# Optimization experiments

Measured on AMD Instinct MI355X. Metric: run time of the kernel, lower is better.

Reference implementation:

```python
import jax, jax.numpy as jnp
import numpy as np

B, S, D, H, DFF = 8, 1024, 1024, 16, 4096
DK = D // H
EPS = 1e-6
NEG = -1e9


def setup_inputs() -> dict:
    key = jax.random.key(0)
    ks = jax.random.split(key, 8)
    x = jax.random.normal(ks[0], (B, S, D), dtype=jnp.float32)
    mask = jnp.ones((B, 1, 1, S), dtype=jnp.int32)
    s = 0.02
    wq = jax.random.normal(ks[1], (D, D), jnp.float32) * s
    wk = jax.random.normal(ks[2], (D, D), jnp.float32) * s
    wv = jax.random.normal(ks[3], (D, D), jnp.float32) * s
    wo = jax.random.normal(ks[4], (D, D), jnp.float32) * s
    bq = jnp.zeros((D,), jnp.float32); bk = jnp.zeros((D,), jnp.float32)
    bv = jnp.zeros((D,), jnp.float32); bo = jnp.zeros((D,), jnp.float32)
    w1 = jax.random.normal(ks[5], (D, DFF), jnp.float32) * s
    b1 = jnp.zeros((DFF,), jnp.float32)
    w2 = jax.random.normal(ks[6], (DFF, D), jnp.float32) * s
    b2 = jnp.zeros((D,), jnp.float32)
    g1 = jnp.array(1.0, jnp.float32); be1 = jnp.array(0.0, jnp.float32)
    g2 = jnp.array(1.0, jnp.float32); be2 = jnp.array(0.0, jnp.float32)
    return dict(x=x, mask=mask, wq=wq, bq=bq, wk=wk, bk=bk, wv=wv, bv=bv,
                wo=wo, bo=bo, w1=w1, b1=b1, w2=w2, b2=b2,
                g1=g1, be1=be1, g2=g2, be2=be2)


def layer_norm(x, gamma, beta):
    # repo quirk: unbiased std (ddof=1), scalar gamma/beta, divide by (std+eps)
    mean = jnp.mean(x, axis=-1, keepdims=True)
    std = jnp.std(x, axis=-1, keepdims=True, ddof=1)
    return gamma * (x - mean) / (std + EPS) + beta


def mha(x, mask, wq, bq, wk, bk, wv, bv, wo, bo):
    q = (x @ wq + bq).reshape(B, S, H, DK).transpose(0, 2, 1, 3)  # bhsd
    k = (x @ wk + bk).reshape(B, S, H, DK).transpose(0, 2, 1, 3)
    v = (x @ wv + bv).reshape(B, S, H, DK).transpose(0, 2, 1, 3)
    scores = jnp.einsum('bhqd,bhkd->bhqk', q, k) / jnp.sqrt(jnp.float32(DK))
    scores = jnp.where(mask == 0, NEG, scores)
    attn = jax.nn.softmax(scores, axis=-1)
    out = jnp.einsum('bhqk,bhkd->bhqd', attn, v)
    out = out.transpose(0, 2, 1, 3).reshape(B, S, D)
    return out @ wo + bo


def reference(x, mask, wq, bq, wk, bk, wv, bv, wo, bo, w1, b1, w2, b2, g1, be1, g2, be2):
    # pre-LN residual: x + sublayer(norm(x)); dropout inert at eval
    x = x + mha(layer_norm(x, g1, be1), mask, wq, bq, wk, bk, wv, bv, wo, bo)
    h = layer_norm(x, g2, be2)
    x = x + (jax.nn.relu(h @ w1 + b1) @ w2 + b2)
    return x
```

## Files before the change

### kernel.cpp

```cpp
#include <hip/hip_runtime.h>
#include <math.h>

typedef __bf16 bf16;
typedef float f32x4 __attribute__((ext_vector_type(4)));
typedef bf16 bf16x8 __attribute__((ext_vector_type(8)));
typedef bf16 bf16x4 __attribute__((ext_vector_type(4)));

#define DEV __device__ __forceinline__

constexpr int Ss = 1024, Dd = 1024;
constexpr float EPSf = 1e-6f;
constexpr float SM_SCALE = 0.125f * 1.4426950408889634f;

DEV void gl_lds16(const void* g, void* l) {
  __builtin_amdgcn_global_load_lds(
      (const __attribute__((address_space(1))) void*)g,
      (__attribute__((address_space(3))) void*)l, 16, 0, 0);
}

__global__ __launch_bounds__(256) void transpose6_k(
    const float* __restrict__ i0, const float* __restrict__ i1,
    const float* __restrict__ i2, const float* __restrict__ i3,
    const float* __restrict__ i4, const float* __restrict__ i5,
    bf16* __restrict__ o0, bf16* __restrict__ o1, bf16* __restrict__ o2,
    bf16* __restrict__ o3, bf16* __restrict__ o4, bf16* __restrict__ o5) {
  __shared__ float t[64 * 65];
  const int bi = blockIdx.x;
  const float* in;
  bf16* out;
  int R, C, local, sh;
  if (bi < 1024) {
    const int j = bi >> 8;
    local = bi & 255; R = 1024; C = 1024; sh = 4;
    in = (j == 0) ? i0 : (j == 1) ? i1 : (j == 2) ? i2 : i3;
    out = (j == 0) ? o0 : (j == 1) ? o1 : (j == 2) ? o2 : o3;
  } else if (bi < 2048) {
    local = bi - 1024; R = 1024; C = 4096; sh = 6; in = i4; out = o4;
  } else {
    local = bi - 2048; R = 4096; C = 1024; sh = 4; in = i5; out = o5;
  }
  const int nx = 1 << sh;
  const int bx = local & (nx - 1), by = local >> sh;
  const int tid = threadIdx.x;
  const int tx = tid & 63, ty = tid >> 6;
  const int r0 = by * 64, c0 = bx * 64;
#pragma unroll
  for (int i = 0; i < 16; i++) {
    int r = ty + i * 4;
    t[r * 65 + tx] = in[(size_t)(r0 + r) * C + c0 + tx];
  }
  __syncthreads();
#pragma unroll
  for (int i = 0; i < 16; i++) {
    int r = ty + i * 4;
    out[(size_t)(c0 + r) * R + r0 + tx] = (bf16)t[tx * 65 + r];
  }
}

__global__ __launch_bounds__(256) void ln_kernel(
    const float* __restrict__ in, bf16* __restrict__ out,
    const float* __restrict__ gp, const float* __restrict__ bp) {
  const int row = blockIdx.x;
  const int tid = threadIdx.x;
  float v[4];
  const float* p = in + (size_t)row * Dd + tid * 4;
#pragma unroll
  for (int i = 0; i < 4; i++) v[i] = p[i];
  float s = v[0] + v[1] + v[2] + v[3];
  float s2 = v[0] * v[0] + v[1] * v[1] + v[2] * v[2] + v[3] * v[3];
#pragma unroll
  for (int m = 1; m < 64; m <<= 1) {
    s += __shfl_xor(s, m, 64);
    s2 += __shfl_xor(s2, m, 64);
  }
  __shared__ float ls[4], ls2[4];
  if ((tid & 63) == 0) {
    ls[tid >> 6] = s;
    ls2[tid >> 6] = s2;
  }
  __syncthreads();
  s = ls[0] + ls[1] + ls[2] + ls[3];
  s2 = ls2[0] + ls2[1] + ls2[2] + ls2[3];
  float mean = s * (1.0f / Dd);
  float var = (s2 - (float)Dd * mean * mean) * (1.0f / (Dd - 1));
  var = fmaxf(var, 0.0f);
  float g = gp[0], be = bp[0];
  float rs = g / (sqrtf(var) + EPSf);
  bf16* q = out + (size_t)row * Dd + tid * 4;
#pragma unroll
  for (int i = 0; i < 4; i++) q[i] = (bf16)((v[i] - mean) * rs + be);
}

template <int EPI, int BK>
__global__ __launch_bounds__(256) void gemm_bt(
    const bf16* __restrict__ A, const bf16* __restrict__ Bt,
    const float* __restrict__ bias, const float* __restrict__ bias2,
    const float* __restrict__ bias3, const float* __restrict__ resid,
    bf16* __restrict__ vtb, void* __restrict__ Cout, int M, int N, int K,
    int sa, int sb) {
  __shared__ __attribute__((aligned(16))) bf16 As[128 * BK];
  __shared__ __attribute__((aligned(16))) bf16 Bs[128 * BK];
  constexpr int CPR = BK / 8;
  constexpr int RPJ = 256 / CPR;
  constexpr int NJ = BK / 16;
  const int tid = threadIdx.x;
  const int ln = tid & 63;
  const int wv = tid >> 6;
  const int wm = wv >> 1, wn = wv & 1;
  const int quad = ln >> 4, l16 = ln & 15;
  const int l7 = l16 & 7;
  const int m0 = blockIdx.y * 128, n0 = blockIdx.x * 128;

  f32x4 acc[4][4];
#pragma unroll
  for (int i = 0; i < 4; i++)
#pragma unroll
    for (int j = 0; j < 4; j++) acc[i][j] = {0.f, 0.f, 0.f, 0.f};

  const int sr = tid / CPR;
  const int sc = (tid & (CPR - 1)) ^ (sr & 7);
  const size_t abase = (size_t)(m0 + sr) * sa + sc * 8;
  const size_t bbase = (size_t)(n0 + sr) * sb + sc * 8;

  for (int k0 = 0; k0 < K; k0 += BK) {
#pragma unroll
    for (int j = 0; j < NJ; j++) {
      gl_lds16(A + abase + (size_t)(j * RPJ) * sa + k0,
               (char*)As + j * 4096 + wv * 1024);
      gl_lds16(Bt + bbase + (size_t)(j * RPJ) * sb + k0,
               (char*)Bs + j * 4096 + wv * 1024);
    }
    __syncthreads();
#pragma unroll
    for (int kh = 0; kh < BK / 32; kh++) {
      bf16x8 af[4], bfr[4];
#pragma unroll
      for (int mi = 0; mi < 4; mi++)
        af[mi] = *(const bf16x8*)&As[(wm * 64 + mi * 16 + l16) * BK +
                                     ((kh * 4 + quad) ^ l7) * 8];
#pragma unroll
      for (int ni = 0; ni < 4; ni++)
        bfr[ni] = *(const bf16x8*)&Bs[(wn * 64 + ni * 16 + l16) * BK +
                                      ((kh * 4 + quad) ^ l7) * 8];
#pragma unroll
      for (int mi = 0; mi < 4; mi++)
#pragma unroll
        for (int ni = 0; ni < 4; ni++)
          acc[mi][ni] = __builtin_amdgcn_mfma_f32_16x16x32_bf16(
              af[mi], bfr[ni], acc[mi][ni], 0, 0, 0);
    }
    __syncthreads();
  }

#pragma unroll
  for (int mi = 0; mi < 4; mi++) {
    const int m = m0 + wm * 64 + mi * 16 + quad * 4;
#pragma unroll
    for (int ni = 0; ni < 4; ni++) {
      const int n = n0 + wn * 64 + ni * 16 + l16;
      float bvl;
      if constexpr (EPI == 4) {
        const int seg = n >> 10;
        const float* bp = (seg == 0) ? bias : (seg == 1) ? bias2 : bias3;
        bvl = bp[n & 1023];
      } else if constexpr (EPI == 3) {
        bvl = 0.0f;
      } else {
        bvl = bias[n];
      }
      if constexpr (EPI == 4) {
        if (n < 2048) {
#pragma unroll
          for (int r = 0; r < 4; r++)
            ((bf16*)Cout)[(size_t)(m + r) * N + n] =
                (bf16)(acc[mi][ni][r] + bvl);
        } else {
          bf16x4 tv;
#pragma unroll
          for (int r = 0; r < 4; r++) tv[r] = (bf16)(acc[mi][ni][r] + bvl);
          const size_t vrow = (size_t)((m >> 10) * 1024 + (n - 2048));
          *(bf16x4*)&vtb[vrow * Ss + (m & 1023)] = tv;
        }
      } else {
#pragma unroll
        for (int r = 0; r < 4; r++) {
          float val = acc[mi][ni][r] + bvl;
          const size_t idx = (size_t)(m + r) * N + n;
          if constexpr (EPI == 1) {
            ((float*)Cout)[idx] = val + resid[idx];
          } else if constexpr (EPI == 2) {
            ((bf16*)Cout)[idx] = (bf16)fmaxf(val, 0.0f);
          } else {
            ((float*)Cout)[idx] = val + resid[idx];
          }
        }
      }
    }
  }
}

__global__ __launch_bounds__(256) void attn_k(
    const bf16* __restrict__ qkv, const bf16* __restrict__ vt,
    const int* __restrict__ mask, bf16* __restrict__ ctx) {
  __shared__ __attribute__((aligned(16))) bf16 Qs[128 * 64];
  __shared__ __attribute__((aligned(16))) bf16 Ks[64 * 64];
  __shared__ __attribute__((aligned(16))) bf16 Vs[64 * 64];
  __shared__ __attribute__((aligned(16))) bf16 Ps[4 * 32 * 64];
  __shared__ float Fm[1024];
  const int tid = threadIdx.x;
  const int ln = tid & 63, w = tid >> 6;
  const int quad = ln >> 4, l16 = ln & 15;
  const int l7 = l16 & 7;
  const int bh = blockIdx.y;
  const int b = bh >> 4, h = bh & 15;
  const int q0 = blockIdx.x * 128;
  const int sr = tid >> 3;
  const int sc = (tid & 7) ^ (sr & 7);

  {
    const int4 mv = *(const int4*)&mask[b * Ss + tid * 4];
    const float ninf = -__builtin_inff();
    Fm[tid * 4 + 0] = mv.x ? 0.0f : ninf;
    Fm[tid * 4 + 1] = mv.y ? 0.0f : ninf;
    Fm[tid * 4 + 2] = mv.z ? 0.0f : ninf;
    Fm[tid * 4 + 3] = mv.w ? 0.0f : ninf;
  }
  {
#pragma unroll
    for (int j = 0; j < 4; j++) {
      const size_t ga =
          (size_t)(b * Ss + q0 + j * 32 + sr) * 3072 + h * 64 + sc * 8;
      gl_lds16(qkv + ga, (char*)Qs + j * 4096 + w * 1024);
    }
  }
  __syncthreads();
  bf16x8 aq[2][2];
#pragma unroll
  for (int qi = 0; qi < 2; qi++)
#pragma unroll
    for (int c = 0; c < 2; c++)
      aq[qi][c] = *(const bf16x8*)&Qs[(w * 32 + qi * 16 + l16) * 64 +
                                      ((c * 4 + quad) ^ l7) * 8];

  f32x4 o[2][4];
#pragma unroll
  for (int qi = 0; qi < 2; qi++)
#pragma unroll
    for (int i = 0; i < 4; i++) o[qi][i] = {0.f, 0.f, 0.f, 0.f};
  f32x4 psum[2] = {{0.f, 0.f, 0.f, 0.f}, {0.f, 0.f, 0.f, 0.f}};

  for (int kk0 = 0; kk0 < Ss; kk0 += 64) {
    {
#pragma unroll
      for (int j = 0; j < 2; j++) {
        const size_t ga = (size_t)(b * Ss + kk0 + j * 32 + sr) * 3072 + 1024 +
                          h * 64 + sc * 8;
        gl_lds16(qkv + ga, (char*)Ks + j * 4096 + w * 1024);
        const size_t gv = (size_t)(bh * 64 + j * 32 + sr) * Ss + kk0 + sc * 8;
        gl_lds16(vt + gv, (char*)Vs + j * 4096 + w * 1024);
      }
    }
    __syncthreads();

    f32x4 st[2][4];
#pragma unroll
    for (int nt = 0; nt < 4; nt++) {
      bf16x8 bk0 = *(const bf16x8*)&Ks[(nt * 16 + l16) * 64 + (quad ^ l7) * 8];
      bf16x8 bk1 =
          *(const bf16x8*)&Ks[(nt * 16 + l16) * 64 + ((4 + quad) ^ l7) * 8];
#pragma unroll
      for (int qi = 0; qi < 2; qi++) {
        f32x4 s = {0.f, 0.f, 0.f, 0.f};
        s = __builtin_amdgcn_mfma_f32_16x16x32_bf16(aq[qi][0], bk0, s, 0, 0, 0);
        s = __builtin_amdgcn_mfma_f32_16x16x32_bf16(aq[qi][1], bk1, s, 0, 0, 0);
        st[qi][nt] = s;
      }
    }
    float fmv[4];
#pragma unroll
    for (int nt = 0; nt < 4; nt++) fmv[nt] = Fm[kk0 + nt * 16 + l16];
#pragma unroll
    for (int qi = 0; qi < 2; qi++)
#pragma unroll
      for (int nt = 0; nt < 4; nt++)
#pragma unroll
        for (int r = 0; r < 4; r++) {
          const float p = exp2f(fmaf(st[qi][nt][r], SM_SCALE, fmv[nt]));
          st[qi][nt][r] = p;
          psum[qi][r] += p;
        }
#pragma unroll
    for (int qi = 0; qi < 2; qi++)
#pragma unroll
      for (int nt = 0; nt < 4; nt++) {
        const int ch = nt * 2 + (l16 >> 3);
#pragma unroll
        for (int r = 0; r < 4; r++) {
          const int pr = qi * 16 + quad * 4 + r;
          Ps[w * 2048 + pr * 64 + (ch ^ (pr & 7)) * 8 + l7] =
              (bf16)st[qi][nt][r];
        }
      }
#pragma unroll
    for (int kh = 0; kh < 2; kh++) {
      bf16x8 bv[4];
#pragma unroll
      for (int dt = 0; dt < 4; dt++)
        bv[dt] = *(const bf16x8*)&Vs[(dt * 16 + l16) * 64 +
                                     ((kh * 4 + quad) ^ l7) * 8];
#pragma unroll
      for (int qi = 0; qi < 2; qi++) {
        bf16x8 ap = *(const bf16x8*)&Ps[w * 2048 + (qi * 16 + l16) * 64 +
                                        ((kh * 4 + quad) ^ l7) * 8];
#pragma unroll
        for (int dt = 0; dt < 4; dt++)
          o[qi][dt] =
              __builtin_amdgcn_mfma_f32_16x16x32_bf16(ap, bv[dt], o[qi][dt],
                                                      0, 0, 0);
      }
    }
    __syncthreads();
  }
#pragma unroll
  for (int qi = 0; qi < 2; qi++)
#pragma unroll
    for (int r = 0; r < 4; r++) {
      float s = psum[qi][r];
#pragma unroll
      for (int m = 1; m < 16; m <<= 1) s += __shfl_xor(s, m, 64);
      psum[qi][r] = s;
    }
#pragma unroll
  for (int qi = 0; qi < 2; qi++) {
    const float inv0 = 1.0f / psum[qi][0], inv1 = 1.0f / psum[qi][1];
    const float inv2 = 1.0f / psum[qi][2], inv3 = 1.0f / psum[qi][3];
#pragma unroll
    for (int dt = 0; dt < 4; dt++) {
      const size_t base =
          (size_t)(b * Ss + q0 + w * 32 + qi * 16 + quad * 4) * Dd + h * 64 +
          dt * 16 + l16;
      ctx[base] = (bf16)(o[qi][dt][0] * inv0);
      ctx[base + Dd] = (bf16)(o[qi][dt][1] * inv1);
      ctx[base + 2 * Dd] = (bf16)(o[qi][dt][2] * inv2);
      ctx[base + 3 * Dd] = (bf16)(o[qi][dt][3] * inv3);
    }
  }
}

extern "C" void kernel_launch(void* const* d_in, const int* in_sizes, int n_in,
                              void* d_out, int out_size, void* d_ws,
                              size_t ws_size, hipStream_t stream) {
  (void)in_sizes; (void)n_in; (void)out_size;
  const float* x = (const float*)d_in[0];
  const int* mask = (const int*)d_in[1];
  const float* wq = (const float*)d_in[2];
  const float* bq = (const float*)d_in[3];
  const float* wk = (const float*)d_in[4];
  const float* bk = (const float*)d_in[5];
  const float* wvw = (const float*)d_in[6];
  const float* bv = (const float*)d_in[7];
  const float* wo = (const float*)d_in[8];
  const float* bo = (const float*)d_in[9];
  const float* w1 = (const float*)d_in[10];
  const float* b1 = (const float*)d_in[11];
  const float* w2 = (const float*)d_in[12];
  const float* b2 = (const float*)d_in[13];
  const float* g1 = (const float*)d_in[14];
  const float* be1 = (const float*)d_in[15];
  const float* g2 = (const float*)d_in[16];
  const float* be2 = (const float*)d_in[17];
  float* out = (float*)d_out;

  char* ws = (char*)d_ws;
  const size_t MB = 1024 * 1024;
  bf16* w1T = (bf16*)(ws + 0 * MB);
  bf16* w2T = (bf16*)(ws + 8 * MB);
  bf16* wqkvT = (bf16*)(ws + 16 * MB);
  bf16* woT = (bf16*)(ws + 22 * MB);
  bf16* lnb = (bf16*)(ws + 24 * MB);
  bf16* qkv = (bf16*)(ws + 40 * MB);
  bf16* vtb = (bf16*)(ws + 88 * MB);
  float* x1 = (float*)(ws + 40 * MB);
  bf16* ctx = lnb;

  dim3 blk(256);
  transpose6_k<<<3072, blk, 0, stream>>>(
      wq, wk, wvw, wo, w1, w2, wqkvT, wqkvT + (size_t)1024 * 1024,
      wqkvT + (size_t)2048 * 1024, woT, w1T, w2T);
  ln_kernel<<<8192, blk, 0, stream>>>(x, lnb, g1, be1);
  gemm_bt<4, 64><<<dim3(24, 64), blk, 0, stream>>>(
      lnb, wqkvT, bq, bk, bv, nullptr, vtb, qkv, 8192, 3072, 1024, 1024, 1024);
  attn_k<<<dim3(8, 128), blk, 0, stream>>>(qkv, vtb, mask, ctx);
  gemm_bt<1, 128><<<dim3(8, 64), blk, 0, stream>>>(
      ctx, woT, bo, nullptr, nullptr, x, nullptr, x1, 8192, 1024, 1024, 1024,
      1024);
  ln_kernel<<<8192, blk, 0, stream>>>(x1, lnb, g2, be2);

  if (ws_size >= 136 * MB) {
    bf16* mid = (bf16*)(ws + 72 * MB);
    gemm_bt<2, 64><<<dim3(32, 64), blk, 0, stream>>>(
        lnb, w1T, b1, nullptr, nullptr, nullptr, nullptr, mid, 8192, 4096,
        1024, 1024, 1024);
    gemm_bt<1, 128><<<dim3(8, 64), blk, 0, stream>>>(
        mid, w2T, b2, nullptr, nullptr, x1, nullptr, out, 8192, 1024, 4096,
        4096, 4096);
  } else {
    bf16* mid = (bf16*)(ws + 72 * MB);
    gemm_bt<2, 64><<<dim3(16, 64), blk, 0, stream>>>(
        lnb, w1T, b1, nullptr, nullptr, nullptr, nullptr, mid, 8192, 2048,
        1024, 1024, 1024);
    gemm_bt<1, 128><<<dim3(8, 64), blk, 0, stream>>>(
        mid, w2T, b2, nullptr, nullptr, x1, nullptr, out, 8192, 1024, 2048,
        2048, 4096);
    gemm_bt<2, 64><<<dim3(16, 64), blk, 0, stream>>>(
        lnb, w1T + (size_t)2048 * 1024, b1 + 2048, nullptr, nullptr, nullptr,
        nullptr, mid, 8192, 2048, 1024, 1024, 1024);
    gemm_bt<3, 128><<<dim3(8, 64), blk, 0, stream>>>(
        mid, w2T + 2048, nullptr, nullptr, nullptr, out, nullptr, out, 8192,
        1024, 2048, 2048, 4096);
  }
}
```

Measured before the change: 510.5 us.

## Stage V-transpose through LDS, compute softmax sum via MFMA, alias attention LDS

The QKV GEMM epilogue for the V segment now writes tiles into swizzled shared memory and then stores coalesced 16-byte rows of the transposed V, replacing scattered 8-byte stores. In attention, the row sum of probabilities is computed with an extra MFMA against a ones vector over the bf16 P tile, removing per-element adds and the final cross-lane shuffle reduction. This also makes the sum match the rounded P actually used. Attention shared memory is merged into one buffer with P aliased over Q to shrink the LDS footprint, and the Q load is issued before the mask setup. The risks are an extra barrier in the GEMM epilogue and a larger MFMA count.

```diff
diff --git a/kernel.cpp b/kernel.cpp
--- a/kernel.cpp
+++ b/kernel.cpp
@@ -98,8 +98,9 @@
     const float* __restrict__ bias3, const float* __restrict__ resid,
     bf16* __restrict__ vtb, void* __restrict__ Cout, int M, int N, int K,
     int sa, int sb) {
-  __shared__ __attribute__((aligned(16))) bf16 As[128 * BK];
-  __shared__ __attribute__((aligned(16))) bf16 Bs[128 * BK];
+  __shared__ __attribute__((aligned(16))) char smem[2 * 128 * BK * 2];
+  bf16* As = (bf16*)smem;
+  bf16* Bs = (bf16*)(smem + 128 * BK * 2);
   constexpr int CPR = BK / 8;
   constexpr int RPJ = 256 / CPR;
   constexpr int NJ = BK / 16;
@@ -152,36 +153,57 @@
     __syncthreads();
   }
 
-#pragma unroll
-  for (int mi = 0; mi < 4; mi++) {
-    const int m = m0 + wm * 64 + mi * 16 + quad * 4;
-#pragma unroll
-    for (int ni = 0; ni < 4; ni++) {
-      const int n = n0 + wn * 64 + ni * 16 + l16;
-      float bvl;
-      if constexpr (EPI == 4) {
-        const int seg = n >> 10;
-        const float* bp = (seg == 0) ? bias : (seg == 1) ? bias2 : bias3;
-        bvl = bp[n & 1023];
-      } else if constexpr (EPI == 3) {
-        bvl = 0.0f;
-      } else {
-        bvl = bias[n];
-      }
-      if constexpr (EPI == 4) {
-        if (n < 2048) {
+  if constexpr (EPI == 4) {
+    if (n0 < 2048) {
+#pragma unroll
+      for (int mi = 0; mi < 4; mi++) {
+        const int m = m0 + wm * 64 + mi * 16 + quad * 4;
+#pragma unroll
+        for (int ni = 0; ni < 4; ni++) {
+          const int n = n0 + wn * 64 + ni * 16 + l16;
+          const float bvl = (n < 1024) ? bias[n] : bias2[n - 1024];
 #pragma unroll
           for (int r = 0; r < 4; r++)
             ((bf16*)Cout)[(size_t)(m + r) * N + n] =
                 (bf16)(acc[mi][ni][r] + bvl);
-        } else {
+        }
+      }
+    } else {
+      bf16* T = (bf16*)smem;
+#pragma unroll
+      for (int mi = 0; mi < 4; mi++) {
+        const int ml = wm * 64 + mi * 16 + quad * 4;
+        const int c = ml >> 3, hf = (ml >> 2) & 1;
+#pragma unroll
+        for (int ni = 0; ni < 4; ni++) {
+          const int nl = wn * 64 + ni * 16 + l16;
+          const float bvl = bias3[(n0 - 2048) + nl];
           bf16x4 tv;
 #pragma unroll
           for (int r = 0; r < 4; r++) tv[r] = (bf16)(acc[mi][ni][r] + bvl);
-          const size_t vrow = (size_t)((m >> 10) * 1024 + (n - 2048));
-          *(bf16x4*)&vtb[vrow * Ss + (m & 1023)] = tv;
+          *(bf16x4*)&T[nl * 128 + ((c ^ (nl & 15)) << 3) + (hf << 2)] = tv;
         }
-      } else {
+      }
+      __syncthreads();
+      const size_t vbase =
+          ((size_t)(m0 >> 10) * 1024 + (n0 - 2048)) * Ss + (m0 & 1023);
+#pragma unroll
+      for (int p = 0; p < 8; p++) {
+        const int row = p * 16 + (tid >> 4);
+        const int k = tid & 15;
+        bf16x8 vv = *(const bf16x8*)&T[row * 128 + ((k ^ (row & 15)) << 3)];
+        *(bf16x8*)&vtb[vbase + (size_t)row * Ss + k * 8] = vv;
+      }
+    }
+  } else {
+#pragma unroll
+    for (int mi = 0; mi < 4; mi++) {
+      const int m = m0 + wm * 64 + mi * 16 + quad * 4;
+#pragma unroll
+      for (int ni = 0; ni < 4; ni++) {
+        const int n = n0 + wn * 64 + ni * 16 + l16;
+        float bvl = 0.0f;
+        if constexpr (EPI != 3) bvl = bias[n];
 #pragma unroll
         for (int r = 0; r < 4; r++) {
           float val = acc[mi][ni][r] + bvl;
@@ -202,11 +224,12 @@
 __global__ __launch_bounds__(256) void attn_k(
     const bf16* __restrict__ qkv, const bf16* __restrict__ vt,
     const int* __restrict__ mask, bf16* __restrict__ ctx) {
-  __shared__ __attribute__((aligned(16))) bf16 Qs[128 * 64];
-  __shared__ __attribute__((aligned(16))) bf16 Ks[64 * 64];
-  __shared__ __attribute__((aligned(16))) bf16 Vs[64 * 64];
-  __shared__ __attribute__((aligned(16))) bf16 Ps[4 * 32 * 64];
-  __shared__ float Fm[1024];
+  __shared__ __attribute__((aligned(16))) char smem[36864];
+  bf16* Qs = (bf16*)smem;
+  bf16* Ks = (bf16*)(smem + 16384);
+  bf16* Vs = (bf16*)(smem + 24576);
+  float* Fm = (float*)(smem + 32768);
+  bf16* Ps = Qs;
   const int tid = threadIdx.x;
   const int ln = tid & 63, w = tid >> 6;
   const int quad = ln >> 4, l16 = ln & 15;
@@ -218,6 +241,14 @@
   const int sc = (tid & 7) ^ (sr & 7);
 
   {
+#pragma unroll
+    for (int j = 0; j < 4; j++) {
+      const size_t ga =
+          (size_t)(b * Ss + q0 + j * 32 + sr) * 3072 + h * 64 + sc * 8;
+      gl_lds16(qkv + ga, (char*)Qs + j * 4096 + w * 1024);
+    }
+  }
+  {
     const int4 mv = *(const int4*)&mask[b * Ss + tid * 4];
     const float ninf = -__builtin_inff();
     Fm[tid * 4 + 0] = mv.x ? 0.0f : ninf;
@@ -225,14 +256,6 @@
     Fm[tid * 4 + 2] = mv.z ? 0.0f : ninf;
     Fm[tid * 4 + 3] = mv.w ? 0.0f : ninf;
   }
-  {
-#pragma unroll
-    for (int j = 0; j < 4; j++) {
-      const size_t ga =
-          (size_t)(b * Ss + q0 + j * 32 + sr) * 3072 + h * 64 + sc * 8;
-      gl_lds16(qkv + ga, (char*)Qs + j * 4096 + w * 1024);
-    }
-  }
   __syncthreads();
   bf16x8 aq[2][2];
 #pragma unroll
@@ -242,12 +265,16 @@
       aq[qi][c] = *(const bf16x8*)&Qs[(w * 32 + qi * 16 + l16) * 64 +
                                       ((c * 4 + quad) ^ l7) * 8];
 
+  bf16x8 ONE;
+#pragma unroll
+  for (int i = 0; i < 8; i++) ONE[i] = (bf16)1.0f;
+
   f32x4 o[2][4];
 #pragma unroll
   for (int qi = 0; qi < 2; qi++)
 #pragma unroll
     for (int i = 0; i < 4; i++) o[qi][i] = {0.f, 0.f, 0.f, 0.f};
-  f32x4 psum[2] = {{0.f, 0.f, 0.f, 0.f}, {0.f, 0.f, 0.f, 0.f}};
+  f32x4 osum[2] = {{0.f, 0.f, 0.f, 0.f}, {0.f, 0.f, 0.f, 0.f}};
 
   for (int kk0 = 0; kk0 < Ss; kk0 += 64) {
     {
@@ -284,11 +311,8 @@
 #pragma unroll
       for (int nt = 0; nt < 4; nt++)
 #pragma unroll
-        for (int r = 0; r < 4; r++) {
-          const float p = exp2f(fmaf(st[qi][nt][r], SM_SCALE, fmv[nt]));
-          st[qi][nt][r] = p;
-          psum[qi][r] += p;
-        }
+        for (int r = 0; r < 4; r++)
+          st[qi][nt][r] = exp2f(fmaf(st[qi][nt][r], SM_SCALE, fmv[nt]));
 #pragma unroll
     for (int qi = 0; qi < 2; qi++)
 #pragma unroll
@@ -317,23 +341,16 @@
           o[qi][dt] =
               __builtin_amdgcn_mfma_f32_16x16x32_bf16(ap, bv[dt], o[qi][dt],
                                                       0, 0, 0);
+        osum[qi] =
+            __builtin_amdgcn_mfma_f32_16x16x32_bf16(ap, ONE, osum[qi], 0, 0, 0);
       }
     }
     __syncthreads();
   }
 #pragma unroll
-  for (int qi = 0; qi < 2; qi++)
-#pragma unroll
-    for (int r = 0; r < 4; r++) {
-      float s = psum[qi][r];
-#pragma unroll
-      for (int m = 1; m < 16; m <<= 1) s += __shfl_xor(s, m, 64);
-      psum[qi][r] = s;
-    }
-#pragma unroll
   for (int qi = 0; qi < 2; qi++) {
-    const float inv0 = 1.0f / psum[qi][0], inv1 = 1.0f / psum[qi][1];
-    const float inv2 = 1.0f / psum[qi][2], inv3 = 1.0f / psum[qi][3];
+    const float inv0 = 1.0f / osum[qi][0], inv1 = 1.0f / osum[qi][1];
+    const float inv2 = 1.0f / osum[qi][2], inv3 = 1.0f / osum[qi][3];
 #pragma unroll
     for (int dt = 0; dt < 4; dt++) {
       const size_t base =
```

Measured after the change: 494.6 us. 3.1% less time.
